# Kernel optimization log

Measured on AMD Instinct MI355X. Metric: run time of the kernel, lower is better.

Reference implementation:

```python
import jax, jax.numpy as jnp
import numpy as np

N_NODES = 20000
N_EDGES = 240000
IN_DIM = 20
SH_DIM = 16  # (lmax+1)^2 with lmax=3
DENOM = 1.0
EPS = 1e-12


def spherical_harmonics_lmax3(v):
    """Real spherical harmonics l=0..3 on unit vectors v: [E,3] -> [E,16]."""
    x, y, z = v[:, 0], v[:, 1], v[:, 2]
    x2, y2, z2 = x * x, y * y, z * z
    sh = [
        jnp.full_like(x, 0.28209479177387814),            # l=0
        0.4886025119029199 * y,                            # l=1, m=-1
        0.4886025119029199 * z,                            # l=1, m=0
        0.4886025119029199 * x,                            # l=1, m=1
        1.0925484305920792 * x * y,                        # l=2, m=-2
        1.0925484305920792 * y * z,                        # l=2, m=-1
        0.31539156525252005 * (3.0 * z2 - 1.0),            # l=2, m=0
        1.0925484305920792 * x * z,                        # l=2, m=1
        0.5462742152960396 * (x2 - y2),                    # l=2, m=2
        0.5900435899266435 * y * (3.0 * x2 - y2),          # l=3, m=-3
        2.890611442640554 * x * y * z,                     # l=3, m=-2
        0.4570457994644658 * y * (5.0 * z2 - 1.0),         # l=3, m=-1
        0.3731763325901154 * z * (5.0 * z2 - 3.0),         # l=3, m=0
        0.4570457994644658 * x * (5.0 * z2 - 1.0),         # l=3, m=1
        1.445305721320277 * z * (x2 - y2),                 # l=3, m=2
        0.5900435899266435 * x * (x2 - 3.0 * y2),          # l=3, m=3
    ]
    return jnp.stack(sh, axis=-1)


def setup_inputs() -> dict:
    key = jax.random.key(0)
    ks = jax.random.split(key, 10)
    x = jax.random.normal(ks[0], (N_NODES, IN_DIM), dtype=jnp.float32)
    positions = jax.random.normal(ks[1], (N_NODES, 3), dtype=jnp.float32)
    edge_index = jax.random.randint(ks[2], (2, N_EDGES), 0, N_NODES, dtype=jnp.int32)
    s = 1.0 / np.sqrt(IN_DIM)
    W_pre = jax.random.uniform(ks[3], (IN_DIM, IN_DIM), jnp.float32, -s, s)
    b_pre = jax.random.uniform(ks[4], (IN_DIM,), jnp.float32, -s, s)
    W_post = jax.random.uniform(ks[5], (IN_DIM, IN_DIM), jnp.float32, -s, s)
    b_post = jax.random.uniform(ks[6], (IN_DIM,), jnp.float32, -s, s)
    W_sc = jax.random.uniform(ks[7], (IN_DIM, IN_DIM), jnp.float32, -s, s)
    b_sc = jax.random.uniform(ks[8], (IN_DIM,), jnp.float32, -s, s)
    return {"x": x, "positions": positions, "edge_index": edge_index,
            "W_pre": W_pre, "b_pre": b_pre, "W_post": W_post, "b_post": b_post,
            "W_sc": W_sc, "b_sc": b_sc}


def reference(x, positions, edge_index, W_pre, b_pre, W_post, b_post, W_sc, b_sc):
    row, col = edge_index[0], edge_index[1]
    # per-edge gather + relative positions
    rel = positions[col] - positions[row]                      # [E,3]
    norm = jnp.sqrt(jnp.sum(rel * rel, axis=-1, keepdims=True) + EPS)
    sh = spherical_harmonics_lmax3(rel / norm)                 # [E,16]
    sender = x[row]                                            # [E,20]
    # equivariant tensor product (outer product over irreps channels)
    tp = (sender[:, :, None] * sh[:, None, :]).reshape(sender.shape[0], IN_DIM * SH_DIM)  # [E,320]
    edge_features = jnp.concatenate([sender, tp], axis=1)      # [E,340]
    # scatter-add aggregation to target nodes
    aggr = jax.ops.segment_sum(edge_features, col, num_segments=N_NODES)  # [N,340]
    # node update MLP + shortcut (math of Layer.update)
    h = x / DENOM
    h = jax.nn.relu(h @ W_pre.T + b_pre)
    h = h @ W_post.T + b_post
    out = x @ W_sc.T + b_sc + h                                # [N,20]
    # aggr is computed (and aggregated) by the original propagate; concat so it stays live
    return jnp.concatenate([out, aggr], axis=1)                # [N,360]
```

## Files before the change

### kernel.cpp

```cpp
#include <hip/hip_runtime.h>
#include <stdint.h>

#define N_NODES 20000
#define N_EDGES 240000
#define IN_DIM  20
#define OUT_DIM 360
#define EPS_F   1e-12f
#define NPART   8
#define CAP_P   16
#define SLOTS   (NPART * CAP_P)
#define EDGE_BLOCKS ((N_EDGES + 255) / 256)
#define MLP_BLOCKS  ((N_NODES + 255) / 256)

typedef _Float16 half8   __attribute__((ext_vector_type(8)));
typedef float    floatx16 __attribute__((ext_vector_type(16)));

__device__ __forceinline__ half8 h8_from_u32(uint32_t u0, uint32_t u1,
                                             uint32_t u2, uint32_t u3) {
    union { uint32_t u[4]; half8 h; } t;
    t.u[0] = u0; t.u[1] = u1; t.u[2] = u2; t.u[3] = u3;
    return t.h;
}

__device__ __forceinline__ uint32_t maskpair(int t, int j) {
    return (t > j ? 0xFFFFu : 0u) | (t > j + 1 ? 0xFFFF0000u : 0u);
}

__device__ __forceinline__ float sh_coeff(int k, float xn, float yn, float zn) {
    const float x2 = xn * xn, y2 = yn * yn, z2 = zn * zn;
    switch (k) {
        case 0:  return 0.28209479177387814f;
        case 1:  return 0.4886025119029199f * yn;
        case 2:  return 0.4886025119029199f * zn;
        case 3:  return 0.4886025119029199f * xn;
        case 4:  return 1.0925484305920792f * xn * yn;
        case 5:  return 1.0925484305920792f * yn * zn;
        case 6:  return 0.31539156525252005f * (3.0f * z2 - 1.0f);
        case 7:  return 1.0925484305920792f * xn * zn;
        case 8:  return 0.5462742152960396f * (x2 - y2);
        case 9:  return 0.5900435899266435f * yn * (3.0f * x2 - y2);
        case 10: return 2.890611442640554f  * xn * yn * zn;
        case 11: return 0.4570457994644658f * yn * (5.0f * z2 - 1.0f);
        case 12: return 0.3731763325901154f * zn * (5.0f * z2 - 3.0f);
        case 13: return 0.4570457994644658f * xn * (5.0f * z2 - 1.0f);
        case 14: return 1.445305721320277f  * zn * (x2 - y2);
        default: return 0.5900435899266435f * xn * (x2 - 3.0f * y2);
    }
}

__global__ __launch_bounds__(256) void bucket_mlp(
    const int* __restrict__ ei,
    const float* __restrict__ x,
    const float* __restrict__ Wpre,  const float* __restrict__ bpre,
    const float* __restrict__ Wpost, const float* __restrict__ bpost,
    const float* __restrict__ Wsc,   const float* __restrict__ bsc,
    int* __restrict__ cnt_pad,
    int* __restrict__ ovf_cnt,
    int* __restrict__ ovf,
    uint16_t* __restrict__ bucket16,
    uint32_t* __restrict__ xpair,
    float* __restrict__ out)
{
    if ((int)blockIdx.x < EDGE_BLOCKS) {
        const int e = (int)(blockIdx.x * 256 + threadIdx.x);
        if (e >= N_EDGES) return;
        const int p = (int)(blockIdx.x & (NPART - 1));
        const int row = ei[e];
        const int col = ei[N_EDGES + e];
        const int slot = atomicAdd(&cnt_pad[((size_t)(p * N_NODES + col)) << 4], 1);
        if (slot >= CAP_P) { ovf[atomicAdd(ovf_cnt, 1)] = e; return; }
        bucket16[col * SLOTS + (p << 4) + slot] = (uint16_t)row;
        return;
    }

    __shared__ float sWpre[IN_DIM * IN_DIM];
    __shared__ float sWpost[IN_DIM * IN_DIM];
    __shared__ float sWsc[IN_DIM * IN_DIM];
    __shared__ float sb[3 * IN_DIM];

    for (int t = (int)threadIdx.x; t < IN_DIM * IN_DIM; t += 256) {
        sWpre[t]  = Wpre[t];
        sWpost[t] = Wpost[t];
        sWsc[t]   = Wsc[t];
    }
    if (threadIdx.x < IN_DIM) {
        sb[threadIdx.x]              = bpre[threadIdx.x];
        sb[IN_DIM + threadIdx.x]     = bpost[threadIdx.x];
        sb[2 * IN_DIM + threadIdx.x] = bsc[threadIdx.x];
    }
    __syncthreads();

    const int i = (int)((blockIdx.x - EDGE_BLOCKS) * 256 + threadIdx.x);
    if (i >= N_NODES) return;

    float xi[IN_DIM], h[IN_DIM];
#pragma unroll
    for (int j = 0; j < IN_DIM; ++j) xi[j] = x[(size_t)i * IN_DIM + j];

#pragma unroll
    for (int j = 0; j < IN_DIM; ++j) {
        const float v = xi[j];
        const _Float16 hh = (_Float16)v;
        const float res = v - (float)hh;
        union { _Float16 f[2]; uint32_t u; } t;
        t.f[0] = hh; t.f[1] = (_Float16)res;
        xpair[(size_t)i * IN_DIM + j] = t.u;
    }

#pragma unroll
    for (int j = 0; j < IN_DIM; ++j) {
        float a = sb[j];
#pragma unroll
        for (int kk = 0; kk < IN_DIM; ++kk) a = fmaf(xi[kk], sWpre[j * IN_DIM + kk], a);
        h[j] = fmaxf(a, 0.0f);
    }
#pragma unroll
    for (int j = 0; j < IN_DIM; ++j) {
        float a = sb[IN_DIM + j] + sb[2 * IN_DIM + j];
#pragma unroll
        for (int kk = 0; kk < IN_DIM; ++kk) {
            a = fmaf(h[kk],  sWpost[j * IN_DIM + kk], a);
            a = fmaf(xi[kk], sWsc[j * IN_DIM + kk],  a);
        }
        out[(size_t)i * OUT_DIM + j] = a;
    }
}

__global__ __launch_bounds__(256) void node_gather(
    const float* __restrict__ x,
    const float* __restrict__ pos,
    const int* __restrict__ ei,
    const int* __restrict__ cnt_pad,
    const uint16_t* __restrict__ bucket16,
    const uint32_t* __restrict__ xpair,
    const int* __restrict__ ovf_cnt,
    const int* __restrict__ ovf,
    float* __restrict__ out)
{
    __shared__ uint16_t shls[4][64][16];

    const int lane  = threadIdx.x & 63;
    const int w     = (int)(threadIdx.x >> 6);
    const int node  = __builtin_amdgcn_readfirstlane(
        (int)((blockIdx.x * blockDim.x + threadIdx.x) >> 6));
    const int col   = lane & 31;
    const int hi    = lane >> 5;
    const int khalf = hi * 8;
    const int rowc  = min(col, IN_DIM - 1);

    int ovf_any = 0;
    int c[NPART];
#pragma unroll
    for (int q = 0; q < NPART; ++q) {
        const int cr = __builtin_amdgcn_readfirstlane(
            cnt_pad[((size_t)(q * N_NODES + node)) << 4]);
        ovf_any |= (cr > CAP_P);
        c[q] = min(cr, CAP_P);
    }
    int pre = 0, pp = 0, base = 0;
#pragma unroll
    for (int q = 0; q < NPART; ++q) {
        if (q >= 1) {
            const int ge = (lane >= pre) ? 1 : 0;
            pp  += ge;
            base = ge ? pre : base;
        }
        pre += c[q];
    }
    const int cnt = min(pre, 64);
    const int s  = min(lane - base, CAP_P - 1);
    const int m  = (pp << 4) + s;

    const int rl = (int)min((uint32_t)bucket16[node * SLOTS + m],
                            (uint32_t)(N_NODES - 1));

    {
        const float pnx = pos[node * 3 + 0];
        const float pny = pos[node * 3 + 1];
        const float pnz = pos[node * 3 + 2];
        const float rx = pnx - pos[rl * 3 + 0];
        const float ry = pny - pos[rl * 3 + 1];
        const float rz = pnz - pos[rl * 3 + 2];
        const float rinv = rsqrtf(rx * rx + ry * ry + rz * rz + EPS_F);
        const float xx = rx * rinv, yy = ry * rinv, zz = rz * rinv;
        const float x2 = xx * xx, y2 = yy * yy, z2 = zz * zz;

        const float sh0  = 0.28209479177387814f;
        const float sh1  = 0.4886025119029199f * yy;
        const float sh2  = 0.4886025119029199f * zz;
        const float sh3  = 0.4886025119029199f * xx;
        const float sh4  = 1.0925484305920792f * xx * yy;
        const float sh5  = 1.0925484305920792f * yy * zz;
        const float sh6  = 0.31539156525252005f * (3.0f * z2 - 1.0f);
        const float sh7  = 1.0925484305920792f * xx * zz;
        const float sh8  = 0.5462742152960396f * (x2 - y2);
        const float sh9  = 0.5900435899266435f * yy * (3.0f * x2 - y2);
        const float sh10 = 2.890611442640554f  * xx * yy * zz;
        const float sh11 = 0.4570457994644658f * yy * (5.0f * z2 - 1.0f);
        const float sh12 = 0.3731763325901154f * zz * (5.0f * z2 - 3.0f);
        const float sh13 = 0.4570457994644658f * xx * (5.0f * z2 - 1.0f);
        const float sh14 = 1.445305721320277f  * zz * (x2 - y2);
        const float sh15 = 0.5900435899266435f * xx * (x2 - 3.0f * y2);

        const half8 v0 = { (_Float16)sh0,  (_Float16)sh1,  (_Float16)sh2,  (_Float16)sh3,
                           (_Float16)sh4,  (_Float16)sh5,  (_Float16)sh6,  (_Float16)sh7 };
        const half8 v1 = { (_Float16)sh8,  (_Float16)sh9,  (_Float16)sh10, (_Float16)sh11,
                           (_Float16)sh12, (_Float16)sh13, (_Float16)sh14, (_Float16)sh15 };
        half8* wp = (half8*)&shls[w][lane][0];
        wp[0] = v0;
        wp[1] = v1;
    }
    __syncthreads();

    floatx16 acc = {0,0,0,0,0,0,0,0,0,0,0,0,0,0,0,0};

    if (cnt > 0) {
        const int nb = (cnt + 15) >> 4;

        for (int b = 0; b < nb; ++b) {
            const int sbase = 16 * b + khalf;

            int rr[8];
#pragma unroll
            for (int j = 0; j < 8; ++j)
                rr[j] = __shfl(rl, sbase + j, 64);
            uint32_t ee[8];
#pragma unroll
            for (int j = 0; j < 8; ++j)
                ee[j] = xpair[(size_t)rr[j] * IN_DIM + rowc];

            uint32_t B0, B1, B2, B3;
            if (col < 16) {
                const uint32_t h0 = shls[w][sbase + 0][col];
                const uint32_t h1 = shls[w][sbase + 1][col];
                const uint32_t h2 = shls[w][sbase + 2][col];
                const uint32_t h3 = shls[w][sbase + 3][col];
                const uint32_t h4 = shls[w][sbase + 4][col];
                const uint32_t h5 = shls[w][sbase + 5][col];
                const uint32_t h6 = shls[w][sbase + 6][col];
                const uint32_t h7 = shls[w][sbase + 7][col];
                B0 = h0 | (h1 << 16);
                B1 = h2 | (h3 << 16);
                B2 = h4 | (h5 << 16);
                B3 = h6 | (h7 << 16);
            } else if (col == 16) {
                B0 = B1 = B2 = B3 = 0x3C003C00u;
            } else {
                B0 = B1 = B2 = B3 = 0u;
            }
            const int rem = cnt - 16 * b;
            if (rem < 16) {
                const int t = rem - khalf;
                B0 &= maskpair(t, 0);
                B1 &= maskpair(t, 2);
                B2 &= maskpair(t, 4);
                B3 &= maskpair(t, 6);
            }

            uint32_t a1u[4], a2u[4];
#pragma unroll
            for (int pq = 0; pq < 4; ++pq) {
                a1u[pq] = (ee[2 * pq] & 0xFFFFu)  | (ee[2 * pq + 1] << 16);
                a2u[pq] = (ee[2 * pq] >> 16)      | (ee[2 * pq + 1] & 0xFFFF0000u);
            }

            const half8 hb  = h8_from_u32(B0, B1, B2, B3);
            const half8 ha1 = h8_from_u32(a1u[0], a1u[1], a1u[2], a1u[3]);
            const half8 ha2 = h8_from_u32(a2u[0], a2u[1], a2u[2], a2u[3]);
            acc = __builtin_amdgcn_mfma_f32_32x32x16_f16(ha1, hb, acc, 0, 0, 0);
            acc = __builtin_amdgcn_mfma_f32_32x32x16_f16(ha2, hb, acc, 0, 0, 0);
        }
    }

    if (ovf_any) {
        const int mm = *ovf_cnt;
        for (int t2 = 0; t2 < mm; ++t2) {
            const int e = ovf[t2];
            if (ei[N_EDGES + e] != node) continue;
            const int row = ei[e];
            const float rx = pos[node * 3 + 0] - pos[row * 3 + 0];
            const float ry = pos[node * 3 + 1] - pos[row * 3 + 1];
            const float rz = pos[node * 3 + 2] - pos[row * 3 + 2];
            const float rinv = rsqrtf(rx * rx + ry * ry + rz * rz + EPS_F);
            float shc;
            if (col < 16)       shc = sh_coeff(col, rx * rinv, ry * rinv, rz * rinv);
            else if (col == 16) shc = 1.0f;
            else                shc = 0.0f;
#pragma unroll
            for (int r = 0; r < 16; ++r) {
                const int rw = ((r & 3) + 8 * (r >> 2)) + 4 * hi;
                if (rw < IN_DIM)
                    acc[r] = fmaf(x[(size_t)row * IN_DIM + rw], shc, acc[r]);
            }
        }
    }

    float* orow = out + (size_t)node * OUT_DIM;
    if (col < 16) {
#pragma unroll
        for (int r = 0; r < 16; ++r) {
            const int rw = ((r & 3) + 8 * (r >> 2)) + 4 * hi;
            if (rw < IN_DIM) orow[2 * IN_DIM + rw * 16 + col] = acc[r];
        }
    } else if (col == 16) {
#pragma unroll
        for (int r = 0; r < 16; ++r) {
            const int rw = ((r & 3) + 8 * (r >> 2)) + 4 * hi;
            if (rw < IN_DIM) orow[IN_DIM + rw] = acc[r];
        }
    }
}

extern "C" void kernel_launch(void* const* d_in, const int* in_sizes, int n_in,
                              void* d_out, int out_size, void* d_ws, size_t ws_size,
                              hipStream_t stream)
{
    const float* x     = (const float*)d_in[0];
    const float* pos   = (const float*)d_in[1];
    const int*   ei    = (const int*)d_in[2];
    const float* Wpre  = (const float*)d_in[3];
    const float* bpre  = (const float*)d_in[4];
    const float* Wpost = (const float*)d_in[5];
    const float* bpost = (const float*)d_in[6];
    const float* Wsc   = (const float*)d_in[7];
    const float* bsc   = (const float*)d_in[8];
    float* out = (float*)d_out;

    char* wp = (char*)d_ws;
    uint16_t* bucket16 = (uint16_t*)wp;   wp += (size_t)N_NODES * SLOTS * 2;
    uint32_t* xpair    = (uint32_t*)wp;   wp += (size_t)N_NODES * IN_DIM * 4;
    int*      cnt_pad  = (int*)wp;        wp += (size_t)NPART * N_NODES * 64;
    int*      ovf_cnt  = (int*)wp;        wp += 4;
    int*      ovf      = (int*)wp;

    hipMemsetAsync(cnt_pad, 0, (size_t)NPART * N_NODES * 64 + 4, stream);

    bucket_mlp<<<EDGE_BLOCKS + MLP_BLOCKS, 256, 0, stream>>>(
        ei, x, Wpre, bpre, Wpost, bpost, Wsc, bsc,
        cnt_pad, ovf_cnt, ovf, bucket16, xpair, out);

    node_gather<<<(N_NODES * 64) / 256, 256, 0, stream>>>(
        x, pos, ei, cnt_pad, bucket16, xpair, ovf_cnt, ovf, out);
}
```

Baseline: 117.5 us.

## Fuse bucketing, MLP and gather into one persistent cooperative kernel

Merges the edge-bucketing/MLP kernel and the per-node gather kernel into one persistent cooperative kernel that uses a grid-wide sync between phases. Grid-stride loops cover the original blocks, and the gather phase reuses the weight shared memory through a union. The aim is to remove the second kernel launch and the inter-kernel drain/ramp gap. In exchange the grid is capped at 1024 blocks, which reduces parallelism in the gather phase, and a grid barrier is added. The previous two-kernel path is kept as a fallback if the cooperative launch fails.

```diff
diff --git a/kernel.cpp b/kernel.cpp
--- a/kernel.cpp
+++ b/kernel.cpp
@@ -1,5 +1,8 @@
 #include <hip/hip_runtime.h>
+#include <hip/hip_cooperative_groups.h>
 #include <stdint.h>
+
+namespace cg = cooperative_groups;
 
 #define N_NODES 20000
 #define N_EDGES 240000
@@ -11,6 +14,8 @@
 #define SLOTS   (NPART * CAP_P)
 #define EDGE_BLOCKS ((N_EDGES + 255) / 256)
 #define MLP_BLOCKS  ((N_NODES + 255) / 256)
+#define P1_BLOCKS   (EDGE_BLOCKS + MLP_BLOCKS)
+#define GATHER_VB   (N_NODES / 4)
 
 typedef _Float16 half8   __attribute__((ext_vector_type(8)));
 typedef float    floatx16 __attribute__((ext_vector_type(16)));
@@ -48,51 +53,22 @@
     }
 }
 
-__global__ __launch_bounds__(256) void bucket_mlp(
-    const int* __restrict__ ei,
-    const float* __restrict__ x,
-    const float* __restrict__ Wpre,  const float* __restrict__ bpre,
-    const float* __restrict__ Wpost, const float* __restrict__ bpost,
-    const float* __restrict__ Wsc,   const float* __restrict__ bsc,
-    int* __restrict__ cnt_pad,
-    int* __restrict__ ovf_cnt,
-    int* __restrict__ ovf,
-    uint16_t* __restrict__ bucket16,
-    uint32_t* __restrict__ xpair,
-    float* __restrict__ out)
-{
-    if ((int)blockIdx.x < EDGE_BLOCKS) {
-        const int e = (int)(blockIdx.x * 256 + threadIdx.x);
-        if (e >= N_EDGES) return;
-        const int p = (int)(blockIdx.x & (NPART - 1));
-        const int row = ei[e];
-        const int col = ei[N_EDGES + e];
-        const int slot = atomicAdd(&cnt_pad[((size_t)(p * N_NODES + col)) << 4], 1);
-        if (slot >= CAP_P) { ovf[atomicAdd(ovf_cnt, 1)] = e; return; }
-        bucket16[col * SLOTS + (p << 4) + slot] = (uint16_t)row;
-        return;
-    }
-
-    __shared__ float sWpre[IN_DIM * IN_DIM];
-    __shared__ float sWpost[IN_DIM * IN_DIM];
-    __shared__ float sWsc[IN_DIM * IN_DIM];
-    __shared__ float sb[3 * IN_DIM];
-
-    for (int t = (int)threadIdx.x; t < IN_DIM * IN_DIM; t += 256) {
-        sWpre[t]  = Wpre[t];
-        sWpost[t] = Wpost[t];
-        sWsc[t]   = Wsc[t];
-    }
-    if (threadIdx.x < IN_DIM) {
-        sb[threadIdx.x]              = bpre[threadIdx.x];
-        sb[IN_DIM + threadIdx.x]     = bpost[threadIdx.x];
-        sb[2 * IN_DIM + threadIdx.x] = bsc[threadIdx.x];
-    }
-    __syncthreads();
-
-    const int i = (int)((blockIdx.x - EDGE_BLOCKS) * 256 + threadIdx.x);
-    if (i >= N_NODES) return;
-
+
+__device__ __forceinline__ void edge_body(int e, int p, const int* __restrict__ ei,
+    int* __restrict__ cnt_pad, int* __restrict__ ovf_cnt, int* __restrict__ ovf,
+    uint16_t* __restrict__ bucket16)
+{
+    const int row = ei[e];
+    const int col = ei[N_EDGES + e];
+    const int slot = atomicAdd(&cnt_pad[((size_t)(p * N_NODES + col)) << 4], 1);
+    if (slot >= CAP_P) { ovf[atomicAdd(ovf_cnt, 1)] = e; return; }
+    bucket16[col * SLOTS + (p << 4) + slot] = (uint16_t)row;
+}
+
+__device__ __forceinline__ void mlp_body(int i,
+    const float* sWpre, const float* sWpost, const float* sWsc, const float* sb,
+    const float* __restrict__ x, uint32_t* __restrict__ xpair, float* __restrict__ out)
+{
     float xi[IN_DIM], h[IN_DIM];
 #pragma unroll
     for (int j = 0; j < IN_DIM; ++j) xi[j] = x[(size_t)i * IN_DIM + j];
@@ -126,23 +102,13 @@
     }
 }
 
-__global__ __launch_bounds__(256) void node_gather(
-    const float* __restrict__ x,
-    const float* __restrict__ pos,
-    const int* __restrict__ ei,
-    const int* __restrict__ cnt_pad,
-    const uint16_t* __restrict__ bucket16,
-    const uint32_t* __restrict__ xpair,
-    const int* __restrict__ ovf_cnt,
-    const int* __restrict__ ovf,
+__device__ __forceinline__ void gather_body(int node, int lane, uint16_t* sh,
+    const float* __restrict__ x, const float* __restrict__ pos,
+    const int* __restrict__ ei, const int* __restrict__ cnt_pad,
+    const uint16_t* __restrict__ bucket16, const uint32_t* __restrict__ xpair,
+    const int* __restrict__ ovf_cnt, const int* __restrict__ ovf,
     float* __restrict__ out)
 {
-    __shared__ uint16_t shls[4][64][16];
-
-    const int lane  = threadIdx.x & 63;
-    const int w     = (int)(threadIdx.x >> 6);
-    const int node  = __builtin_amdgcn_readfirstlane(
-        (int)((blockIdx.x * blockDim.x + threadIdx.x) >> 6));
     const int col   = lane & 31;
     const int hi    = lane >> 5;
     const int khalf = hi * 8;
@@ -173,14 +139,10 @@
 
     const int rl = (int)min((uint32_t)bucket16[node * SLOTS + m],
                             (uint32_t)(N_NODES - 1));
-
     {
-        const float pnx = pos[node * 3 + 0];
-        const float pny = pos[node * 3 + 1];
-        const float pnz = pos[node * 3 + 2];
-        const float rx = pnx - pos[rl * 3 + 0];
-        const float ry = pny - pos[rl * 3 + 1];
-        const float rz = pnz - pos[rl * 3 + 2];
+        const float rx = pos[node * 3 + 0] - pos[rl * 3 + 0];
+        const float ry = pos[node * 3 + 1] - pos[rl * 3 + 1];
+        const float rz = pos[node * 3 + 2] - pos[rl * 3 + 2];
         const float rinv = rsqrtf(rx * rx + ry * ry + rz * rz + EPS_F);
         const float xx = rx * rinv, yy = ry * rinv, zz = rz * rinv;
         const float x2 = xx * xx, y2 = yy * yy, z2 = zz * zz;
@@ -206,17 +168,15 @@
                            (_Float16)sh4,  (_Float16)sh5,  (_Float16)sh6,  (_Float16)sh7 };
         const half8 v1 = { (_Float16)sh8,  (_Float16)sh9,  (_Float16)sh10, (_Float16)sh11,
                            (_Float16)sh12, (_Float16)sh13, (_Float16)sh14, (_Float16)sh15 };
-        half8* wp = (half8*)&shls[w][lane][0];
+        half8* wp = (half8*)&sh[lane * 16];
         wp[0] = v0;
         wp[1] = v1;
     }
-    __syncthreads();
 
     floatx16 acc = {0,0,0,0,0,0,0,0,0,0,0,0,0,0,0,0};
 
     if (cnt > 0) {
         const int nb = (cnt + 15) >> 4;
-
         for (int b = 0; b < nb; ++b) {
             const int sbase = 16 * b + khalf;
 
@@ -231,14 +191,14 @@
 
             uint32_t B0, B1, B2, B3;
             if (col < 16) {
-                const uint32_t h0 = shls[w][sbase + 0][col];
-                const uint32_t h1 = shls[w][sbase + 1][col];
-                const uint32_t h2 = shls[w][sbase + 2][col];
-                const uint32_t h3 = shls[w][sbase + 3][col];
-                const uint32_t h4 = shls[w][sbase + 4][col];
-                const uint32_t h5 = shls[w][sbase + 5][col];
-                const uint32_t h6 = shls[w][sbase + 6][col];
-                const uint32_t h7 = shls[w][sbase + 7][col];
+                const uint32_t h0 = sh[(sbase + 0) * 16 + col];
+                const uint32_t h1 = sh[(sbase + 1) * 16 + col];
+                const uint32_t h2 = sh[(sbase + 2) * 16 + col];
+                const uint32_t h3 = sh[(sbase + 3) * 16 + col];
+                const uint32_t h4 = sh[(sbase + 4) * 16 + col];
+                const uint32_t h5 = sh[(sbase + 5) * 16 + col];
+                const uint32_t h6 = sh[(sbase + 6) * 16 + col];
+                const uint32_t h7 = sh[(sbase + 7) * 16 + col];
                 B0 = h0 | (h1 << 16);
                 B1 = h2 | (h3 << 16);
                 B2 = h4 | (h5 << 16);
@@ -311,6 +271,107 @@
     }
 }
 
+__global__ __launch_bounds__(256) void fused(
+    const float* __restrict__ x, const float* __restrict__ pos,
+    const int* __restrict__ ei,
+    const float* __restrict__ Wpre,  const float* __restrict__ bpre,
+    const float* __restrict__ Wpost, const float* __restrict__ bpost,
+    const float* __restrict__ Wsc,   const float* __restrict__ bsc,
+    int* __restrict__ cnt_pad, int* __restrict__ ovf_cnt, int* __restrict__ ovf,
+    uint16_t* __restrict__ bucket16, uint32_t* __restrict__ xpair,
+    float* __restrict__ out)
+{
+    __shared__ union {
+        float w[1260];
+        uint16_t shls[4][64][16];
+    } sm;
+    const int tid = (int)threadIdx.x;
+
+    for (int t = tid; t < 400; t += 256) {
+        sm.w[t]        = Wpre[t];
+        sm.w[400 + t]  = Wpost[t];
+        sm.w[800 + t]  = Wsc[t];
+    }
+    if (tid < IN_DIM) {
+        sm.w[1200 + tid]              = bpre[tid];
+        sm.w[1200 + IN_DIM + tid]     = bpost[tid];
+        sm.w[1200 + 2 * IN_DIM + tid] = bsc[tid];
+    }
+    __syncthreads();
+
+    for (int blk = (int)blockIdx.x; blk < P1_BLOCKS; blk += (int)gridDim.x) {
+        if (blk < EDGE_BLOCKS) {
+            const int e = blk * 256 + tid;
+            if (e < N_EDGES)
+                edge_body(e, blk & (NPART - 1), ei, cnt_pad, ovf_cnt, ovf, bucket16);
+        } else {
+            const int i = (blk - EDGE_BLOCKS) * 256 + tid;
+            if (i < N_NODES)
+                mlp_body(i, sm.w, sm.w + 400, sm.w + 800, sm.w + 1200, x, xpair, out);
+        }
+    }
+
+    __threadfence();
+    cg::this_grid().sync();
+
+    const int lane = tid & 63;
+    const int w    = tid >> 6;
+    uint16_t* sh = &sm.shls[w][0][0];
+    for (int vb = (int)blockIdx.x; vb < GATHER_VB; vb += (int)gridDim.x) {
+        const int node = __builtin_amdgcn_readfirstlane(vb * 4 + w);
+        gather_body(node, lane, sh, x, pos, ei, cnt_pad, bucket16, xpair,
+                    ovf_cnt, ovf, out);
+    }
+}
+
+__global__ __launch_bounds__(256) void bucket_mlp(
+    const int* __restrict__ ei, const float* __restrict__ x,
+    const float* __restrict__ Wpre,  const float* __restrict__ bpre,
+    const float* __restrict__ Wpost, const float* __restrict__ bpost,
+    const float* __restrict__ Wsc,   const float* __restrict__ bsc,
+    int* __restrict__ cnt_pad, int* __restrict__ ovf_cnt, int* __restrict__ ovf,
+    uint16_t* __restrict__ bucket16, uint32_t* __restrict__ xpair,
+    float* __restrict__ out)
+{
+    if ((int)blockIdx.x < EDGE_BLOCKS) {
+        const int e = (int)(blockIdx.x * 256 + threadIdx.x);
+        if (e < N_EDGES)
+            edge_body(e, (int)(blockIdx.x & (NPART - 1)), ei, cnt_pad, ovf_cnt, ovf, bucket16);
+        return;
+    }
+    __shared__ float smw[1260];
+    for (int t = (int)threadIdx.x; t < 400; t += 256) {
+        smw[t]       = Wpre[t];
+        smw[400 + t] = Wpost[t];
+        smw[800 + t] = Wsc[t];
+    }
+    if (threadIdx.x < IN_DIM) {
+        smw[1200 + threadIdx.x]              = bpre[threadIdx.x];
+        smw[1200 + IN_DIM + threadIdx.x]     = bpost[threadIdx.x];
+        smw[1200 + 2 * IN_DIM + threadIdx.x] = bsc[threadIdx.x];
+    }
+    __syncthreads();
+    const int i = (int)((blockIdx.x - EDGE_BLOCKS) * 256 + threadIdx.x);
+    if (i < N_NODES)
+        mlp_body(i, smw, smw + 400, smw + 800, smw + 1200, x, xpair, out);
+}
+
+__global__ __launch_bounds__(256) void node_gather(
+    const float* __restrict__ x, const float* __restrict__ pos,
+    const int* __restrict__ ei, const int* __restrict__ cnt_pad,
+    const uint16_t* __restrict__ bucket16, const uint32_t* __restrict__ xpair,
+    const int* __restrict__ ovf_cnt, const int* __restrict__ ovf,
+    float* __restrict__ out)
+{
+    __shared__ uint16_t shls[4][64][16];
+    const int lane = (int)(threadIdx.x & 63);
+    const int w    = (int)(threadIdx.x >> 6);
+    const int node = __builtin_amdgcn_readfirstlane(
+        (int)((blockIdx.x * blockDim.x + threadIdx.x) >> 6));
+    gather_body(node, lane, &shls[w][0][0], x, pos, ei, cnt_pad, bucket16, xpair,
+                ovf_cnt, ovf, out);
+}
+
 extern "C" void kernel_launch(void* const* d_in, const int* in_sizes, int n_in,
                               void* d_out, int out_size, void* d_ws, size_t ws_size,
                               hipStream_t stream)
@@ -335,10 +396,39 @@
 
     hipMemsetAsync(cnt_pad, 0, (size_t)NPART * N_NODES * 64 + 4, stream);
 
-    bucket_mlp<<<EDGE_BLOCKS + MLP_BLOCKS, 256, 0, stream>>>(
-        ei, x, Wpre, bpre, Wpost, bpost, Wsc, bsc,
-        cnt_pad, ovf_cnt, ovf, bucket16, xpair, out);
-
-    node_gather<<<(N_NODES * 64) / 256, 256, 0, stream>>>(
-        x, pos, ei, cnt_pad, bucket16, xpair, ovf_cnt, ovf, out);
-}
+    static int coop_grid = -2;
+    if (coop_grid == -2) {
+        int bpc = 0;
+        if (hipOccupancyMaxActiveBlocksPerMultiprocessor(
+                &bpc, (const void*)fused, 256, 0) == hipSuccess && bpc > 0) {
+            long g = (long)bpc * 256;
+            if (g > 1024) g = 1024;
+            coop_grid = (int)g;
+        } else {
+            coop_grid = -1;
+        }
+    }
+
+    bool done = false;
+    if (coop_grid > 0) {
+        void* args[] = { (void*)&x, (void*)&pos, (void*)&ei,
+                         (void*)&Wpre, (void*)&bpre, (void*)&Wpost, (void*)&bpost,
+                         (void*)&Wsc, (void*)&bsc,
+                         (void*)&cnt_pad, (void*)&ovf_cnt, (void*)&ovf,
+                         (void*)&bucket16, (void*)&xpair, (void*)&out };
+        if (hipLaunchCooperativeKernel((const void*)fused, dim3(coop_grid), dim3(256),
+                                       args, 0, stream) == hipSuccess) {
+            done = true;
+        } else {
+            coop_grid = -1;
+        }
+    }
+
+    if (!done) {
+        bucket_mlp<<<EDGE_BLOCKS + MLP_BLOCKS, 256, 0, stream>>>(
+            ei, x, Wpre, bpre, Wpost, bpost, Wsc, bsc,
+            cnt_pad, ovf_cnt, ovf, bucket16, xpair, out);
+        node_gather<<<(N_NODES * 64) / 256, 256, 0, stream>>>(
+            x, pos, ei, cnt_pad, bucket16, xpair, ovf_cnt, ovf, out);
+    }
+}
```

Result: no change. 117.8 us (+0.2%).

## Replace partitioned padded edge counters with single per-node bucket of 64

Applied to the files above, without the earlier changes.

Edge bucketing drops the 8-way partitioned, 64-byte-padded counters and uses one dense per-node counter with a 64-slot bucket. This shrinks the memset and the counter reads, and removes the prefix-scan lane mapping in the gather kernel. The cost is more atomic contention on the shared counters, which were padded before to avoid it. The overflow path is moved into a noinline function to lower register pressure, and a __syncthreads is dropped (shared staging appears per-wave).

```diff
diff --git a/kernel.cpp b/kernel.cpp
--- a/kernel.cpp
+++ b/kernel.cpp
@@ -6,9 +6,7 @@
 #define IN_DIM  20
 #define OUT_DIM 360
 #define EPS_F   1e-12f
-#define NPART   8
-#define CAP_P   16
-#define SLOTS   (NPART * CAP_P)
+#define CAP     64
 #define EDGE_BLOCKS ((N_EDGES + 255) / 256)
 #define MLP_BLOCKS  ((N_NODES + 255) / 256)
 
@@ -26,7 +24,7 @@
     return (t > j ? 0xFFFFu : 0u) | (t > j + 1 ? 0xFFFF0000u : 0u);
 }
 
-__device__ __forceinline__ float sh_coeff(int k, float xn, float yn, float zn) {
+__device__ float sh_coeff(int k, float xn, float yn, float zn) {
     const float x2 = xn * xn, y2 = yn * yn, z2 = zn * zn;
     switch (k) {
         case 0:  return 0.28209479177387814f;
@@ -48,13 +46,41 @@
     }
 }
 
+__device__ __noinline__ floatx16 ovf_accum(floatx16 acc, int node, int col, int hi,
+    const float* __restrict__ x, const float* __restrict__ pos,
+    const int* __restrict__ ei, const int* __restrict__ ovf_cnt,
+    const int* __restrict__ ovf)
+{
+    const int mm = *ovf_cnt;
+    for (int t2 = 0; t2 < mm; ++t2) {
+        const int e = ovf[t2];
+        if (ei[N_EDGES + e] != node) continue;
+        const int row = ei[e];
+        const float rx = pos[node * 3 + 0] - pos[row * 3 + 0];
+        const float ry = pos[node * 3 + 1] - pos[row * 3 + 1];
+        const float rz = pos[node * 3 + 2] - pos[row * 3 + 2];
+        const float rinv = rsqrtf(rx * rx + ry * ry + rz * rz + EPS_F);
+        float shc;
+        if (col < 16)       shc = sh_coeff(col, rx * rinv, ry * rinv, rz * rinv);
+        else if (col == 16) shc = 1.0f;
+        else                shc = 0.0f;
+#pragma unroll
+        for (int r = 0; r < 16; ++r) {
+            const int rw = ((r & 3) + 8 * (r >> 2)) + 4 * hi;
+            if (rw < IN_DIM)
+                acc[r] = fmaf(x[(size_t)row * IN_DIM + rw], shc, acc[r]);
+        }
+    }
+    return acc;
+}
+
 __global__ __launch_bounds__(256) void bucket_mlp(
     const int* __restrict__ ei,
     const float* __restrict__ x,
     const float* __restrict__ Wpre,  const float* __restrict__ bpre,
     const float* __restrict__ Wpost, const float* __restrict__ bpost,
     const float* __restrict__ Wsc,   const float* __restrict__ bsc,
-    int* __restrict__ cnt_pad,
+    int* __restrict__ counts,
     int* __restrict__ ovf_cnt,
     int* __restrict__ ovf,
     uint16_t* __restrict__ bucket16,
@@ -64,34 +90,34 @@
     if ((int)blockIdx.x < EDGE_BLOCKS) {
         const int e = (int)(blockIdx.x * 256 + threadIdx.x);
         if (e >= N_EDGES) return;
-        const int p = (int)(blockIdx.x & (NPART - 1));
         const int row = ei[e];
         const int col = ei[N_EDGES + e];
-        const int slot = atomicAdd(&cnt_pad[((size_t)(p * N_NODES + col)) << 4], 1);
-        if (slot >= CAP_P) { ovf[atomicAdd(ovf_cnt, 1)] = e; return; }
-        bucket16[col * SLOTS + (p << 4) + slot] = (uint16_t)row;
+        const int slot = atomicAdd(&counts[col], 1);
+        if (slot >= CAP) { ovf[atomicAdd(ovf_cnt, 1)] = e; return; }
+        bucket16[col * CAP + slot] = (uint16_t)row;
         return;
     }
 
-    __shared__ float sWpre[IN_DIM * IN_DIM];
-    __shared__ float sWpost[IN_DIM * IN_DIM];
-    __shared__ float sWsc[IN_DIM * IN_DIM];
-    __shared__ float sb[3 * IN_DIM];
-
-    for (int t = (int)threadIdx.x; t < IN_DIM * IN_DIM; t += 256) {
-        sWpre[t]  = Wpre[t];
-        sWpost[t] = Wpost[t];
-        sWsc[t]   = Wsc[t];
+    __shared__ float smw[1260];
+    for (int t = (int)threadIdx.x; t < 400; t += 256) {
+        smw[t]       = Wpre[t];
+        smw[400 + t] = Wpost[t];
+        smw[800 + t] = Wsc[t];
     }
     if (threadIdx.x < IN_DIM) {
-        sb[threadIdx.x]              = bpre[threadIdx.x];
-        sb[IN_DIM + threadIdx.x]     = bpost[threadIdx.x];
-        sb[2 * IN_DIM + threadIdx.x] = bsc[threadIdx.x];
+        smw[1200 + threadIdx.x]              = bpre[threadIdx.x];
+        smw[1200 + IN_DIM + threadIdx.x]     = bpost[threadIdx.x];
+        smw[1200 + 2 * IN_DIM + threadIdx.x] = bsc[threadIdx.x];
     }
     __syncthreads();
 
     const int i = (int)((blockIdx.x - EDGE_BLOCKS) * 256 + threadIdx.x);
     if (i >= N_NODES) return;
+
+    const float* sWpre  = smw;
+    const float* sWpost = smw + 400;
+    const float* sWsc   = smw + 800;
+    const float* sb     = smw + 1200;
 
     float xi[IN_DIM], h[IN_DIM];
 #pragma unroll
@@ -130,7 +156,7 @@
     const float* __restrict__ x,
     const float* __restrict__ pos,
     const int* __restrict__ ei,
-    const int* __restrict__ cnt_pad,
+    const int* __restrict__ counts,
     const uint16_t* __restrict__ bucket16,
     const uint32_t* __restrict__ xpair,
     const int* __restrict__ ovf_cnt,
@@ -139,7 +165,7 @@
 {
     __shared__ uint16_t shls[4][64][16];
 
-    const int lane  = threadIdx.x & 63;
+    const int lane  = (int)(threadIdx.x & 63);
     const int w     = (int)(threadIdx.x >> 6);
     const int node  = __builtin_amdgcn_readfirstlane(
         (int)((blockIdx.x * blockDim.x + threadIdx.x) >> 6));
@@ -148,39 +174,15 @@
     const int khalf = hi * 8;
     const int rowc  = min(col, IN_DIM - 1);
 
-    int ovf_any = 0;
-    int c[NPART];
-#pragma unroll
-    for (int q = 0; q < NPART; ++q) {
-        const int cr = __builtin_amdgcn_readfirstlane(
-            cnt_pad[((size_t)(q * N_NODES + node)) << 4]);
-        ovf_any |= (cr > CAP_P);
-        c[q] = min(cr, CAP_P);
-    }
-    int pre = 0, pp = 0, base = 0;
-#pragma unroll
-    for (int q = 0; q < NPART; ++q) {
-        if (q >= 1) {
-            const int ge = (lane >= pre) ? 1 : 0;
-            pp  += ge;
-            base = ge ? pre : base;
-        }
-        pre += c[q];
-    }
-    const int cnt = min(pre, 64);
-    const int s  = min(lane - base, CAP_P - 1);
-    const int m  = (pp << 4) + s;
-
-    const int rl = (int)min((uint32_t)bucket16[node * SLOTS + m],
-                            (uint32_t)(N_NODES - 1));
-
-    {
-        const float pnx = pos[node * 3 + 0];
-        const float pny = pos[node * 3 + 1];
-        const float pnz = pos[node * 3 + 2];
-        const float rx = pnx - pos[rl * 3 + 0];
-        const float ry = pny - pos[rl * 3 + 1];
-        const float rz = pnz - pos[rl * 3 + 2];
+    const int cnt_raw = __builtin_amdgcn_readfirstlane(counts[node]);
+    const int cnt = min(cnt_raw, CAP);
+
+    int rl = 0;
+    if (lane < cnt) {
+        rl = (int)bucket16[node * CAP + lane];
+        const float rx = pos[node * 3 + 0] - pos[rl * 3 + 0];
+        const float ry = pos[node * 3 + 1] - pos[rl * 3 + 1];
+        const float rz = pos[node * 3 + 2] - pos[rl * 3 + 2];
         const float rinv = rsqrtf(rx * rx + ry * ry + rz * rz + EPS_F);
         const float xx = rx * rinv, yy = ry * rinv, zz = rz * rinv;
         const float x2 = xx * xx, y2 = yy * yy, z2 = zz * zz;
@@ -210,13 +212,11 @@
         wp[0] = v0;
         wp[1] = v1;
     }
-    __syncthreads();
 
     floatx16 acc = {0,0,0,0,0,0,0,0,0,0,0,0,0,0,0,0};
 
     if (cnt > 0) {
         const int nb = (cnt + 15) >> 4;
-
         for (int b = 0; b < nb; ++b) {
             const int sbase = 16 * b + khalf;
 
@@ -224,10 +224,12 @@
 #pragma unroll
             for (int j = 0; j < 8; ++j)
                 rr[j] = __shfl(rl, sbase + j, 64);
+
             uint32_t ee[8];
 #pragma unroll
             for (int j = 0; j < 8; ++j)
-                ee[j] = xpair[(size_t)rr[j] * IN_DIM + rowc];
+                ee[j] = (sbase + j < cnt && col < IN_DIM)
+                      ? xpair[(size_t)rr[j] * IN_DIM + rowc] : 0u;
 
             uint32_t B0, B1, B2, B3;
             if (col < 16) {
@@ -272,28 +274,8 @@
         }
     }
 
-    if (ovf_any) {
-        const int mm = *ovf_cnt;
-        for (int t2 = 0; t2 < mm; ++t2) {
-            const int e = ovf[t2];
-            if (ei[N_EDGES + e] != node) continue;
-            const int row = ei[e];
-            const float rx = pos[node * 3 + 0] - pos[row * 3 + 0];
-            const float ry = pos[node * 3 + 1] - pos[row * 3 + 1];
-            const float rz = pos[node * 3 + 2] - pos[row * 3 + 2];
-            const float rinv = rsqrtf(rx * rx + ry * ry + rz * rz + EPS_F);
-            float shc;
-            if (col < 16)       shc = sh_coeff(col, rx * rinv, ry * rinv, rz * rinv);
-            else if (col == 16) shc = 1.0f;
-            else                shc = 0.0f;
-#pragma unroll
-            for (int r = 0; r < 16; ++r) {
-                const int rw = ((r & 3) + 8 * (r >> 2)) + 4 * hi;
-                if (rw < IN_DIM)
-                    acc[r] = fmaf(x[(size_t)row * IN_DIM + rw], shc, acc[r]);
-            }
-        }
-    }
+    if (cnt_raw > CAP)
+        acc = ovf_accum(acc, node, col, hi, x, pos, ei, ovf_cnt, ovf);
 
     float* orow = out + (size_t)node * OUT_DIM;
     if (col < 16) {
@@ -327,18 +309,18 @@
     float* out = (float*)d_out;
 
     char* wp = (char*)d_ws;
-    uint16_t* bucket16 = (uint16_t*)wp;   wp += (size_t)N_NODES * SLOTS * 2;
+    uint16_t* bucket16 = (uint16_t*)wp;   wp += (size_t)N_NODES * CAP * 2;
     uint32_t* xpair    = (uint32_t*)wp;   wp += (size_t)N_NODES * IN_DIM * 4;
-    int*      cnt_pad  = (int*)wp;        wp += (size_t)NPART * N_NODES * 64;
+    int*      counts   = (int*)wp;        wp += (size_t)N_NODES * 4;
     int*      ovf_cnt  = (int*)wp;        wp += 4;
     int*      ovf      = (int*)wp;
 
-    hipMemsetAsync(cnt_pad, 0, (size_t)NPART * N_NODES * 64 + 4, stream);
+    hipMemsetAsync(counts, 0, (size_t)(N_NODES + 1) * sizeof(int), stream);
 
     bucket_mlp<<<EDGE_BLOCKS + MLP_BLOCKS, 256, 0, stream>>>(
         ei, x, Wpre, bpre, Wpost, bpost, Wsc, bsc,
-        cnt_pad, ovf_cnt, ovf, bucket16, xpair, out);
+        counts, ovf_cnt, ovf, bucket16, xpair, out);
 
     node_gather<<<(N_NODES * 64) / 256, 256, 0, stream>>>(
-        x, pos, ei, cnt_pad, bucket16, xpair, ovf_cnt, ovf, out);
-}
+        x, pos, ei, counts, bucket16, xpair, ovf_cnt, ovf, out);
+}
```

Result: no change. 118.2 us (+0.6%).
